# Kernel tuning notes

Hardware: AMD Instinct MI355X
Metric: run time of the kernel (lower is better)

Reference implementation:

```python
import jax, jax.numpy as jnp
import numpy as np

HIDDEN = 1024
N_HEADS = 16
N_LAYERS = 10
LOCAL_K = 3
TOKEN_T, TOKEN_H, TOKEN_W = 4, 16, 16
PATCH_SIZE = 2
LATENT_C = 16
TOKEN_DIM = LATENT_C * PATCH_SIZE * PATCH_SIZE  # 64
TOKEN_IN = TOKEN_DIM + 1                        # 65
N_TOKENS = TOKEN_T * TOKEN_H * TOKEN_W          # 1024
B = 1
HEAD_DIM = HIDDEN // N_HEADS
LN_EPS = 1e-5


def layer_norm(x, w, b):
    m = x.mean(-1, keepdims=True)
    v = ((x - m) ** 2).mean(-1, keepdims=True)
    return (x - m) * jax.lax.rsqrt(v + LN_EPS) * w + b


def patchify(lat):
    Bx, T, C, H, W = lat.shape
    ph, pw = H // PATCH_SIZE, W // PATCH_SIZE
    x = lat.reshape(Bx, T, C, ph, PATCH_SIZE, pw, PATCH_SIZE)
    x = x.transpose(0, 1, 3, 5, 2, 4, 6)
    return x.reshape(Bx, T * ph * pw, C * PATCH_SIZE * PATCH_SIZE)


def unpatchify(tok):
    Bx = tok.shape[0]
    C = TOKEN_DIM // (PATCH_SIZE * PATCH_SIZE)
    x = tok.reshape(Bx, TOKEN_T, TOKEN_H, TOKEN_W, C, PATCH_SIZE, PATCH_SIZE)
    x = x.transpose(0, 1, 4, 2, 5, 3, 6)
    return x.reshape(Bx, TOKEN_T, C, TOKEN_H * PATCH_SIZE, TOKEN_W * PATCH_SIZE)


def gather_neighbors(kv):
    # kv: (B, N, 2D) -> (B, N, 27, 2D), 3x3x3 zero-padded neighborhoods
    Bx, Nx, D2 = kv.shape
    pad = LOCAL_K // 2
    x = kv.reshape(Bx, TOKEN_T, TOKEN_H, TOKEN_W, D2)
    x = jnp.pad(x, ((0, 0), (pad, pad), (pad, pad), (pad, pad), (0, 0)))
    sl = [x[:, dt:dt + TOKEN_T, dh:dh + TOKEN_H, dw:dw + TOKEN_W]
          for dt in range(LOCAL_K) for dh in range(LOCAL_K) for dw in range(LOCAL_K)]
    nb = jnp.stack(sl, axis=4)  # (B,T,H,W,27,2D)
    return nb.reshape(Bx, Nx, LOCAL_K ** 3, D2)


def local_attention(x, qkv_w, out_w):
    Bx, Nx, D = x.shape
    H, d = N_HEADS, HEAD_DIM
    qkv = x @ qkv_w                       # (B,N,3D)
    q, k, v = jnp.split(qkv, 3, axis=-1)
    kv_nb = gather_neighbors(jnp.concatenate([k, v], axis=-1))  # (B,N,27,2D)
    k_nb, v_nb = jnp.split(kv_nb, 2, axis=-1)
    q = q.reshape(Bx, Nx, H, d)
    k_nb = k_nb.reshape(Bx, Nx, LOCAL_K ** 3, H, d)
    v_nb = v_nb.reshape(Bx, Nx, LOCAL_K ** 3, H, d)
    scores = jnp.einsum('bnhd,bnkhd->bnhk', q, k_nb) / np.sqrt(d).astype(np.float32)
    probs = jax.nn.softmax(scores, axis=-1)
    out = jnp.einsum('bnhk,bnkhd->bnhd', probs, v_nb).reshape(Bx, Nx, D)
    return out @ out_w


def global_attention(x, mask_flat, qkv_w, out_w):
    # Each masked query attends to all N keys; math identical to the
    # gather/SDPA/scatter in the original (per-query attention is independent),
    # realized as full attention masked to zero at unmasked positions.
    Bx, Nx, D = x.shape
    H, d = N_HEADS, HEAD_DIM
    qkv = x @ qkv_w
    q, k, v = jnp.split(qkv, 3, axis=-1)
    q = q.reshape(Bx, Nx, H, d)
    k = k.reshape(Bx, Nx, H, d)
    v = v.reshape(Bx, Nx, H, d)
    scores = jnp.einsum('bqhd,bkhd->bhqk', q, k) / np.sqrt(d).astype(np.float32)
    probs = jax.nn.softmax(scores, axis=-1)
    out = jnp.einsum('bhqk,bkhd->bqhd', probs, v).reshape(Bx, Nx, D)
    out = out @ out_w
    return out * mask_flat[..., None].astype(out.dtype)


def setup_inputs() -> dict:
    key = jax.random.key(0)
    ks = jax.random.split(key, 24)
    s = 0.02
    L, D = N_LAYERS, HIDDEN
    inp = {
        'latents': jax.random.normal(ks[0], (B, TOKEN_T, LATENT_C, TOKEN_H * PATCH_SIZE, TOKEN_W * PATCH_SIZE), jnp.float32),
        'token_mask': jax.random.uniform(ks[1], (B, TOKEN_T, TOKEN_H, TOKEN_W)) < 0.1,
        'input_proj_w': jax.random.normal(ks[2], (TOKEN_IN, D), jnp.float32) * s,
        'input_proj_b': jnp.zeros((D,), jnp.float32),
        'emb_t': jax.random.normal(ks[3], (TOKEN_T, D), jnp.float32) * s,
        'emb_h': jax.random.normal(ks[4], (TOKEN_H, D), jnp.float32) * s,
        'emb_w': jax.random.normal(ks[5], (TOKEN_W, D), jnp.float32) * s,
        'ln_local_w': jnp.ones((L, D), jnp.float32),
        'ln_local_b': jnp.zeros((L, D), jnp.float32),
        'ln_global_w': jnp.ones((L, D), jnp.float32),
        'ln_global_b': jnp.zeros((L, D), jnp.float32),
        'ln_ffn_w': jnp.ones((L, D), jnp.float32),
        'ln_ffn_b': jnp.zeros((L, D), jnp.float32),
        'local_qkv_w': jax.random.normal(ks[6], (L, D, 3 * D), jnp.float32) * s,
        'local_out_w': jax.random.normal(ks[7], (L, D, D), jnp.float32) * s,
        'global_qkv_w': jax.random.normal(ks[8], (L, D, 3 * D), jnp.float32) * s,
        'global_out_w': jax.random.normal(ks[9], (L, D, D), jnp.float32) * s,
        'ffn_w1': jax.random.normal(ks[10], (L, D, 4 * D), jnp.float32) * s,
        'ffn_b1': jnp.zeros((L, 4 * D), jnp.float32),
        'ffn_w2': jax.random.normal(ks[11], (L, 4 * D, D), jnp.float32) * s,
        'ffn_b2': jnp.zeros((L, D), jnp.float32),
        'final_ln_w': jnp.ones((D,), jnp.float32),
        'final_ln_b': jnp.zeros((D,), jnp.float32),
        # original zero-inits output_proj; use small random so the test is non-trivial
        'out_proj_w': jax.random.normal(ks[12], (D, TOKEN_DIM), jnp.float32) * s,
        'out_proj_b': jnp.zeros((TOKEN_DIM,), jnp.float32),
    }
    return inp


def reference(latents, token_mask, input_proj_w, input_proj_b, emb_t, emb_h, emb_w,
              ln_local_w, ln_local_b, ln_global_w, ln_global_b, ln_ffn_w, ln_ffn_b,
              local_qkv_w, local_out_w, global_qkv_w, global_out_w,
              ffn_w1, ffn_b1, ffn_w2, ffn_b2, final_ln_w, final_ln_b,
              out_proj_w, out_proj_b):
    Bx = latents.shape[0]
    mask_flat = token_mask.reshape(Bx, -1)
    tokens = patchify(latents)                       # (B, N, TOKEN_DIM)
    flag = mask_flat[..., None].astype(tokens.dtype)
    x = jnp.concatenate([tokens, flag], axis=-1) @ input_proj_w + input_proj_b

    tt, hh, ww = jnp.meshgrid(jnp.arange(TOKEN_T), jnp.arange(TOKEN_H), jnp.arange(TOKEN_W), indexing='ij')
    pos = emb_t[tt.reshape(-1)] + emb_h[hh.reshape(-1)] + emb_w[ww.reshape(-1)]
    x = x + pos[None]

    for l in range(N_LAYERS):
        x = x + local_attention(layer_norm(x, ln_local_w[l], ln_local_b[l]), local_qkv_w[l], local_out_w[l])
        x = x + global_attention(layer_norm(x, ln_global_w[l], ln_global_b[l]), mask_flat, global_qkv_w[l], global_out_w[l])
        h = layer_norm(x, ln_ffn_w[l], ln_ffn_b[l])
        h = jax.nn.gelu(h @ ffn_w1[l] + ffn_b1[l], approximate=False) @ ffn_w2[l] + ffn_b2[l]
        x = x + h

    delta = layer_norm(x, final_ln_w, final_ln_b) @ out_proj_w + out_proj_b
    return unpatchify(tokens + delta)
```

## Files before the change

kernel.cpp:

```cpp
#include <hip/hip_runtime.h>
#include <hip/hip_bf16.h>
#include <math.h>

typedef __bf16 bf16;
typedef __bf16 bf16x8 __attribute__((ext_vector_type(8)));
typedef __bf16 bf16x4 __attribute__((ext_vector_type(4)));
typedef float  f32x4 __attribute__((ext_vector_type(4)));
typedef unsigned int u32x4 __attribute__((ext_vector_type(4)));

#define NTOK 1024
#define HID  1024
#define NH   16
#define HD   64
#define NL   10
#define QCMAX 256

__global__ __launch_bounds__(256)
void wtrans_k(const float* __restrict__ W, bf16* __restrict__ Wt, int K, int N)
{
    __shared__ bf16 tile[64][72];
    const long mofs = (long)blockIdx.z * K * N;
    const float* Ws = W + mofs;
    bf16* Wo = Wt + mofs;
    const int n0 = blockIdx.x * 64, k0 = blockIdx.y * 64;
    const int t = threadIdx.x;
    {
        const int r = t >> 2, cc = (t & 3) * 16;
        const float* src = Ws + (long)(k0 + r) * N + n0 + cc;
#pragma unroll
        for (int i = 0; i < 2; ++i) {
            f32x4 a = *(const f32x4*)(src + i * 8);
            f32x4 b = *(const f32x4*)(src + i * 8 + 4);
            bf16x8 w;
            w[0]=(bf16)a.x; w[1]=(bf16)a.y; w[2]=(bf16)a.z; w[3]=(bf16)a.w;
            w[4]=(bf16)b.x; w[5]=(bf16)b.y; w[6]=(bf16)b.z; w[7]=(bf16)b.w;
            *(bf16x8*)&tile[r][cc + i * 8] = w;
        }
    }
    __syncthreads();
    {
        const int n = t >> 2, kc = (t & 3) * 16;
        bf16x8 o0, o1;
#pragma unroll
        for (int j = 0; j < 8; ++j) { o0[j] = tile[kc + j][n]; o1[j] = tile[kc + 8 + j][n]; }
        bf16* dst = Wo + (long)(n0 + n) * K + k0 + kc;
        *(bf16x8*)dst = o0;
        *(bf16x8*)(dst + 8) = o1;
    }
}

template<int BM, int BN, int KSPLIT>
__global__ __launch_bounds__(256)
void gemm_k(const bf16* __restrict__ A, int lda, long bsA,
            const bf16* __restrict__ Bt, int ldb, long bsB,
            float* __restrict__ Cf, int ldc, long bsC,
            int K)
{
    constexpr int WC  = (BM == 128) ? 2 : 4;
    constexpr int WTN = BN / WC;
    constexpr int NF  = WTN / 16;
    __shared__ bf16 Al[2][BM * 32];
    __shared__ bf16 Bl[2][BN * 32];

    const int t    = threadIdx.x;
    const int lane = t & 63;
    const int wv   = t >> 6;
    const int wr   = wv / WC, wc = wv % WC;
    const int lrow = lane & 15, lk = lane >> 4;
    const int n0   = blockIdx.x * BN;
    const int m0   = blockIdx.y * BM;
    const int ks   = (KSPLIT > 1) ? (blockIdx.z % KSPLIT) : 0;
    const int bz   = (KSPLIT > 1) ? (blockIdx.z / KSPLIT) : blockIdx.z;
    const int Kc   = K / KSPLIT;

    const bf16* Ab = A  + bsA * bz + (long)ks * Kc;
    const bf16* Bb = Bt + bsB * bz + (long)ks * Kc;

    f32x4 acc[4][NF];
#pragma unroll
    for (int m = 0; m < 4; ++m)
#pragma unroll
        for (int n = 0; n < NF; ++n) acc[m][n] = f32x4{0.f, 0.f, 0.f, 0.f};

    const int sr = t >> 2, sc = (t & 3) * 8;

    auto stage = [&](int buf, int kk) {
#pragma unroll
        for (int i = 0; i < BM / 64; ++i)
            __builtin_amdgcn_global_load_lds(
                (const __attribute__((address_space(1))) void*)(Ab + (long)(m0 + sr + i * 64) * lda + kk + sc),
                (__attribute__((address_space(3))) void*)(&Al[buf][i * 2048 + t * 8]), 16, 0, 0);
#pragma unroll
        for (int i = 0; i < BN / 64; ++i)
            __builtin_amdgcn_global_load_lds(
                (const __attribute__((address_space(1))) void*)(Bb + (long)(n0 + sr + i * 64) * ldb + kk + sc),
                (__attribute__((address_space(3))) void*)(&Bl[buf][i * 2048 + t * 8]), 16, 0, 0);
    };

    stage(0, 0);
    __syncthreads();
    int cur = 0;
    for (int k0 = 0; k0 < Kc; k0 += 32) {
        if (k0 + 32 < Kc) stage(cur ^ 1, k0 + 32);
        bf16x8 af[4], bfv[NF];
#pragma unroll
        for (int m = 0; m < 4; ++m)
            af[m] = *(const bf16x8*)&Al[cur][(wr * 64 + m * 16 + lrow) * 32 + lk * 8];
#pragma unroll
        for (int n = 0; n < NF; ++n)
            bfv[n] = *(const bf16x8*)&Bl[cur][(wc * WTN + n * 16 + lrow) * 32 + lk * 8];
#pragma unroll
        for (int m = 0; m < 4; ++m)
#pragma unroll
            for (int n = 0; n < NF; ++n)
                acc[m][n] = __builtin_amdgcn_mfma_f32_16x16x32_bf16(af[m], bfv[n], acc[m][n], 0, 0, 0);
        __syncthreads();
        cur ^= 1;
    }

    float* Co = Cf + bsC * blockIdx.z;
#pragma unroll
    for (int m = 0; m < 4; ++m)
#pragma unroll
        for (int n = 0; n < NF; ++n) {
            const int c = n0 + wc * WTN + n * 16 + lrow;
#pragma unroll
            for (int q = 0; q < 4; ++q) {
                const int r = m0 + wr * 64 + m * 16 + lk * 4 + q;
                Co[(long)r * ldc + c] = acc[m][n][q];
            }
        }
}

template<int NS, bool BIAS, bool SCATTER>
__global__ __launch_bounds__(256)
void ln_add_k(float* __restrict__ x, const float* __restrict__ parts, long pstride,
              const float* __restrict__ bias, const int* __restrict__ rmap,
              const float* __restrict__ w, const float* __restrict__ b,
              bf16* __restrict__ o)
{
    int row  = blockIdx.x * 4 + (threadIdx.x >> 6);
    int lane = threadIdx.x & 63;
    f32x4* xr = (f32x4*)(x + (long)row * HID) + lane * 4;
    f32x4 v[4];
#pragma unroll
    for (int i = 0; i < 4; ++i) v[i] = xr[i];

    if (NS > 0) {
        int prow = SCATTER ? rmap[row] : row;
        if (!SCATTER || prow >= 0) {
            const float* pp = parts + (long)prow * 1024 + lane * 16;
#pragma unroll
            for (int ksi = 0; ksi < NS; ++ksi) {
                const f32x4* q = (const f32x4*)(pp + (long)ksi * pstride);
#pragma unroll
                for (int i = 0; i < 4; ++i) v[i] += q[i];
            }
            if (BIAS) {
                const f32x4* bb = (const f32x4*)bias + lane * 4;
#pragma unroll
                for (int i = 0; i < 4; ++i) v[i] += bb[i];
            }
#pragma unroll
            for (int i = 0; i < 4; ++i) xr[i] = v[i];
        }
    }

    float s = 0.f;
#pragma unroll
    for (int i = 0; i < 4; ++i) s += v[i].x + v[i].y + v[i].z + v[i].w;
    for (int m = 32; m; m >>= 1) s += __shfl_xor(s, m);
    float mean = s * (1.f / 1024.f);
    f32x4 d[4];
    float ss = 0.f;
#pragma unroll
    for (int i = 0; i < 4; ++i) {
        d[i] = v[i] - mean;
        ss += d[i].x * d[i].x + d[i].y * d[i].y + d[i].z * d[i].z + d[i].w * d[i].w;
    }
    for (int m = 32; m; m >>= 1) ss += __shfl_xor(ss, m);
    float rs = rsqrtf(ss * (1.f / 1024.f) + 1e-5f);
    const f32x4* wp = (const f32x4*)w + lane * 4;
    const f32x4* bp = (const f32x4*)b + lane * 4;
    bf16x8 o0, o1;
#pragma unroll
    for (int i = 0; i < 4; ++i) {
        f32x4 wv = wp[i], bv = bp[i];
        f32x4 e;
        e.x = d[i].x * rs * wv.x + bv.x; e.y = d[i].y * rs * wv.y + bv.y;
        e.z = d[i].z * rs * wv.z + bv.z; e.w = d[i].w * rs * wv.w + bv.w;
        if (i < 2) { o0[i*4+0]=(bf16)e.x; o0[i*4+1]=(bf16)e.y; o0[i*4+2]=(bf16)e.z; o0[i*4+3]=(bf16)e.w; }
        else       { int k=(i-2)*4; o1[k+0]=(bf16)e.x; o1[k+1]=(bf16)e.y; o1[k+2]=(bf16)e.z; o1[k+3]=(bf16)e.w; }
    }
    bf16* op = o + (long)row * HID + lane * 16;
    *(bf16x8*)op = o0;
    *(bf16x8*)(op + 8) = o1;
}

__global__ __launch_bounds__(256)
void red2_k(const float* __restrict__ p, float* __restrict__ out, int n4)
{
    int i = blockIdx.x * 256 + threadIdx.x;
    const f32x4* a = (const f32x4*)p;
    const f32x4* b = a + n4;
    ((f32x4*)out)[i] = a[i] + b[i];
}

__global__ __launch_bounds__(256)
void red_gelu_k(const float* __restrict__ p, const float* __restrict__ bias,
                bf16* __restrict__ out)
{
    int i = blockIdx.x * 256 + threadIdx.x;
    f32x4 a = ((const f32x4*)p)[i];
    f32x4 c = ((const f32x4*)(p + 4194304))[i];
    f32x4 bb = ((const f32x4*)bias)[i & 1023];
    f32x4 u = a + c + bb;
    bf16x4 o;
    o[0] = (bf16)(0.5f * u.x * (1.f + erff(u.x * 0.70710678118654752f)));
    o[1] = (bf16)(0.5f * u.y * (1.f + erff(u.y * 0.70710678118654752f)));
    o[2] = (bf16)(0.5f * u.z * (1.f + erff(u.z * 0.70710678118654752f)));
    o[3] = (bf16)(0.5f * u.w * (1.f + erff(u.w * 0.70710678118654752f)));
    ((bf16x4*)out)[i] = o;
}

__global__ __launch_bounds__(256)
void red4pv_k(const float* __restrict__ p, bf16* __restrict__ Oc)
{
    int i = blockIdx.x * 256 + threadIdx.x;
    int d4 = (i & 15) * 4;
    int r  = (i >> 4) & 255;
    int h  = i >> 12;
    const float* base = p + (long)(h * 4) * 16384 + r * 64 + d4;
    f32x4 s = *(const f32x4*)base;
    s += *(const f32x4*)(base + 16384);
    s += *(const f32x4*)(base + 32768);
    s += *(const f32x4*)(base + 49152);
    bf16x4 o;
    o[0] = (bf16)s.x; o[1] = (bf16)s.y; o[2] = (bf16)s.z; o[3] = (bf16)s.w;
    *(bf16x4*)(Oc + (long)r * 1024 + h * 64 + d4) = o;
}

__global__ __launch_bounds__(256)
void lattn_k(const float* __restrict__ qkv, bf16* __restrict__ ao)
{
    int w    = blockIdx.x * 4 + (threadIdx.x >> 6);
    int lane = threadIdx.x & 63;
    int n = w >> 4, h = w & 15;
    int tt = n >> 8, hh = (n >> 4) & 15, ww = n & 15;

    int nj = -1;
    float dotv = 0.f;
    if (lane < 27) {
        int dt = lane / 9 - 1, dh = (lane % 9) / 3 - 1, dw = lane % 3 - 1;
        int t2 = tt + dt, h2 = hh + dh, w2 = ww + dw;
        if (t2 >= 0 && t2 < 4 && h2 >= 0 && h2 < 16 && w2 >= 0 && w2 < 16)
            nj = (t2 << 8) | (h2 << 4) | w2;
    }
    if (nj >= 0) {
        const f32x4* qp = (const f32x4*)(qkv + (long)n * 3072 + h * 64);
        const f32x4* kp = (const f32x4*)(qkv + (long)nj * 3072 + 1024 + h * 64);
#pragma unroll
        for (int i = 0; i < 16; ++i) {
            f32x4 q4 = qp[i], k4 = kp[i];
            dotv += q4.x * k4.x + q4.y * k4.y + q4.z * k4.z + q4.w * k4.w;
        }
    }
    float sc = (lane < 27) ? dotv * 0.125f : -3.0e38f;
    float mx = sc;
    for (int m = 32; m; m >>= 1) mx = fmaxf(mx, __shfl_xor(mx, m));
    float e = (lane < 27) ? __expf(sc - mx) : 0.f;
    float s = e;
    for (int m = 32; m; m >>= 1) s += __shfl_xor(s, m);
    float p = e / s;

    float acc = 0.f;
    for (int j = 0; j < 27; ++j) {
        float pj = __shfl(p, j);
        int  njj = __shfl(nj, j);
        if (njj >= 0) acc += pj * qkv[(long)njj * 3072 + 2048 + h * 64 + lane];
    }
    ao[(long)n * 1024 + h * 64 + lane] = (bf16)acc;
}

__global__ void compact_k(const int* __restrict__ mask, int* __restrict__ qidx,
                          int* __restrict__ rmap)
{
    int lane = threadIdx.x;
    int total = 0;
    for (int base = 0; base < 1024; base += 64) {
        int m = (mask[base + lane] != 0) ? 1 : 0;
        unsigned long long bal = __ballot(m);
        int pos = total + (int)__popcll(bal & ((1ull << lane) - 1ull));
        int ok = (m && pos < QCMAX);
        if (ok) qidx[pos] = base + lane;
        rmap[base + lane] = ok ? pos : -1;
        total += (int)__popcll(bal);
    }
    for (int i = total + lane; i < QCMAX; i += 64) qidx[i] = -1;
}

__global__ __launch_bounds__(256)
void qbuild_k(const float* __restrict__ qkv, const int* __restrict__ qidx,
              bf16* __restrict__ Qc)
{
    const int h = blockIdx.y;
    const int t = threadIdx.x;
    const int r = blockIdx.x * 64 + (t >> 2), dc = (t & 3) * 16;
    const int q = qidx[r];
    bf16x8 o0, o1;
    if (q >= 0) {
        const f32x4* src = (const f32x4*)(qkv + (long)q * 3072 + h * 64 + dc);
#pragma unroll
        for (int i = 0; i < 2; ++i) {
            f32x4 a = src[i * 2] * 0.125f, b = src[i * 2 + 1] * 0.125f;
            bf16x8 w;
            w[0]=(bf16)a.x; w[1]=(bf16)a.y; w[2]=(bf16)a.z; w[3]=(bf16)a.w;
            w[4]=(bf16)b.x; w[5]=(bf16)b.y; w[6]=(bf16)b.z; w[7]=(bf16)b.w;
            if (i == 0) o0 = w; else o1 = w;
        }
    } else {
#pragma unroll
        for (int j = 0; j < 8; ++j) { o0[j] = (bf16)0.f; o1[j] = (bf16)0.f; }
    }
    bf16* dst = Qc + (long)h * (QCMAX * 64) + (long)r * 64 + dc;
    *(bf16x8*)dst = o0;
    *(bf16x8*)(dst + 8) = o1;
}

__global__ __launch_bounds__(256)
void kvbuild_k(const float* __restrict__ qkv, bf16* __restrict__ Kh,
               bf16* __restrict__ Vt)
{
    __shared__ bf16 vt[64][72];
    const int h = blockIdx.y;
    const int k0 = blockIdx.x * 64;
    const int t = threadIdx.x;
    {
        const int r = t >> 2, dc = (t & 3) * 16;
        const float* kp = qkv + (long)(k0 + r) * 3072 + 1024 + h * 64 + dc;
        const float* vp = kp + 1024;
        bf16x8 ko0, ko1;
#pragma unroll
        for (int i = 0; i < 2; ++i) {
            f32x4 a = *(const f32x4*)(kp + i * 8);
            f32x4 b = *(const f32x4*)(kp + i * 8 + 4);
            bf16x8 w;
            w[0]=(bf16)a.x; w[1]=(bf16)a.y; w[2]=(bf16)a.z; w[3]=(bf16)a.w;
            w[4]=(bf16)b.x; w[5]=(bf16)b.y; w[6]=(bf16)b.z; w[7]=(bf16)b.w;
            if (i == 0) ko0 = w; else ko1 = w;
        }
        bf16* kd = Kh + (long)h * (NTOK * 64) + (long)(k0 + r) * 64 + dc;
        *(bf16x8*)kd = ko0;
        *(bf16x8*)(kd + 8) = ko1;
#pragma unroll
        for (int i = 0; i < 2; ++i) {
            f32x4 a = *(const f32x4*)(vp + i * 8);
            f32x4 b = *(const f32x4*)(vp + i * 8 + 4);
            bf16x8 w;
            w[0]=(bf16)a.x; w[1]=(bf16)a.y; w[2]=(bf16)a.z; w[3]=(bf16)a.w;
            w[4]=(bf16)b.x; w[5]=(bf16)b.y; w[6]=(bf16)b.z; w[7]=(bf16)b.w;
            *(bf16x8*)&vt[r][dc + i * 8] = w;
        }
    }
    __syncthreads();
    {
        const int d = t >> 2, kc = (t & 3) * 16;
        bf16x8 o0, o1;
#pragma unroll
        for (int j = 0; j < 8; ++j) { o0[j] = vt[kc + j][d]; o1[j] = vt[kc + 8 + j][d]; }
        bf16* dst = Vt + (long)h * (64 * NTOK) + (long)d * NTOK + k0 + kc;
        *(bf16x8*)dst = o0;
        *(bf16x8*)(dst + 8) = o1;
    }
}

__global__ __launch_bounds__(256)
void softmax_k(const float* __restrict__ S, bf16* __restrict__ P)
{
    int row  = blockIdx.x * 4 + (threadIdx.x >> 6);
    int lane = threadIdx.x & 63;
    const f32x4* sp = (const f32x4*)(S + (long)row * 1024) + lane * 4;
    f32x4 v[4];
#pragma unroll
    for (int i = 0; i < 4; ++i) v[i] = sp[i];
    float mx = -3.0e38f;
#pragma unroll
    for (int i = 0; i < 4; ++i)
        mx = fmaxf(mx, fmaxf(fmaxf(v[i].x, v[i].y), fmaxf(v[i].z, v[i].w)));
    for (int m = 32; m; m >>= 1) mx = fmaxf(mx, __shfl_xor(mx, m));
    f32x4 ev[4];
    float sum = 0.f;
#pragma unroll
    for (int i = 0; i < 4; ++i) {
        ev[i].x = __expf(v[i].x - mx); ev[i].y = __expf(v[i].y - mx);
        ev[i].z = __expf(v[i].z - mx); ev[i].w = __expf(v[i].w - mx);
        sum += ev[i].x + ev[i].y + ev[i].z + ev[i].w;
    }
    for (int m = 32; m; m >>= 1) sum += __shfl_xor(sum, m);
    float inv = 1.f / sum;
    bf16x8 o0, o1;
#pragma unroll
    for (int i = 0; i < 4; ++i) {
        f32x4 e = ev[i] * inv;
        if (i < 2) { o0[i*4+0]=(bf16)e.x; o0[i*4+1]=(bf16)e.y; o0[i*4+2]=(bf16)e.z; o0[i*4+3]=(bf16)e.w; }
        else       { int k=(i-2)*4; o1[k+0]=(bf16)e.x; o1[k+1]=(bf16)e.y; o1[k+2]=(bf16)e.z; o1[k+3]=(bf16)e.w; }
    }
    bf16* op = P + (long)row * 1024 + lane * 16;
    *(bf16x8*)op = o0;
    *(bf16x8*)(op + 8) = o1;
}

__global__ __launch_bounds__(256)
void prep_k(const float* __restrict__ lat, const int* __restrict__ mask,
            const float* __restrict__ Wi, const float* __restrict__ bi,
            const float* __restrict__ et, const float* __restrict__ eh,
            const float* __restrict__ ew,
            float* __restrict__ x, float* __restrict__ tokens)
{
    __shared__ float tl[16][65];
    int t = threadIdx.x;
    int n0 = blockIdx.x * 16;
    for (int idx = t; idx < 16 * 65; idx += 256) {
        int ti = idx / 65, d = idx % 65;
        int n = n0 + ti;
        int tt = n >> 8, hh = (n >> 4) & 15, wwi = n & 15;
        float v;
        if (d < 64) {
            int c = d >> 2, ph = (d >> 1) & 1, pw = d & 1;
            v = lat[(((long)tt * 16 + c) * 32 + hh * 2 + ph) * 32 + wwi * 2 + pw];
            tokens[(long)n * 64 + d] = v;
        } else {
            v = mask[n] ? 1.f : 0.f;
        }
        tl[ti][d] = v;
    }
    __syncthreads();
    f32x4 acc[16];
#pragma unroll
    for (int i = 0; i < 16; ++i) acc[i] = f32x4{0.f, 0.f, 0.f, 0.f};
    for (int d = 0; d < 65; ++d) {
        f32x4 wv = *(const f32x4*)(Wi + (long)d * 1024 + t * 4);
#pragma unroll
        for (int ti = 0; ti < 16; ++ti) acc[ti] += tl[ti][d] * wv;
    }
    f32x4 bb = *(const f32x4*)(bi + t * 4);
    for (int ti = 0; ti < 16; ++ti) {
        int n = n0 + ti;
        int tt = n >> 8, hh = (n >> 4) & 15, wwi = n & 15;
        f32x4 pos = *(const f32x4*)(et + (long)tt * 1024 + t * 4)
                  + *(const f32x4*)(eh + (long)hh * 1024 + t * 4)
                  + *(const f32x4*)(ew + (long)wwi * 1024 + t * 4);
        *(f32x4*)(x + (long)n * 1024 + t * 4) = acc[ti] + bb + pos;
    }
}

__global__ __launch_bounds__(256)
void final_k(const bf16* __restrict__ xn, const float* __restrict__ OW,
             const float* __restrict__ ob, const float* __restrict__ tokens,
             float* __restrict__ out)
{
    __shared__ bf16 xl[8][1024];
    __shared__ float part[4][8][64];
    int t = threadIdx.x;
    int n0 = blockIdx.x * 8;
    for (int i = t; i < 1024; i += 256)
        ((u32x4*)xl)[i] = ((const u32x4*)(xn + (long)n0 * 1024))[i];
    __syncthreads();
    int j = t & 63, s = t >> 6;
    float acc[8] = {0.f, 0.f, 0.f, 0.f, 0.f, 0.f, 0.f, 0.f};
    for (int k = s * 256; k < s * 256 + 256; ++k) {
        float w = OW[(long)k * 64 + j];
#pragma unroll
        for (int ti = 0; ti < 8; ++ti) acc[ti] += (float)xl[ti][k] * w;
    }
    for (int ti = 0; ti < 8; ++ti) part[s][ti][j] = acc[ti];
    __syncthreads();
    if (s == 0) {
        for (int ti = 0; ti < 8; ++ti) {
            int n = n0 + ti;
            float v = part[0][ti][j] + part[1][ti][j] + part[2][ti][j] + part[3][ti][j]
                    + ob[j] + tokens[(long)n * 64 + j];
            int tt = n >> 8, hh = (n >> 4) & 15, wwi = n & 15;
            int c = j >> 2, ph = (j >> 1) & 1, pw = j & 1;
            out[(((long)tt * 16 + c) * 32 + hh * 2 + ph) * 32 + wwi * 2 + pw] = v;
        }
    }
}

extern "C" void kernel_launch(void* const* d_in, const int* in_sizes, int n_in,
                              void* d_out, int out_size, void* d_ws, size_t ws_size,
                              hipStream_t stream)
{
    const float* latents = (const float*)d_in[0];
    const int*   mask    = (const int*)d_in[1];
    const float* ipw  = (const float*)d_in[2];
    const float* ipb  = (const float*)d_in[3];
    const float* et   = (const float*)d_in[4];
    const float* eh   = (const float*)d_in[5];
    const float* ew   = (const float*)d_in[6];
    const float* lnlw = (const float*)d_in[7];
    const float* lnlb = (const float*)d_in[8];
    const float* lngw = (const float*)d_in[9];
    const float* lngb = (const float*)d_in[10];
    const float* lnfw = (const float*)d_in[11];
    const float* lnfb = (const float*)d_in[12];
    const float* lqkv = (const float*)d_in[13];
    const float* lout = (const float*)d_in[14];
    const float* gqkv = (const float*)d_in[15];
    const float* gout = (const float*)d_in[16];
    const float* w1   = (const float*)d_in[17];
    const float* b1   = (const float*)d_in[18];
    const float* w2   = (const float*)d_in[19];
    const float* b2   = (const float*)d_in[20];
    const float* flw  = (const float*)d_in[21];
    const float* flb  = (const float*)d_in[22];
    const float* opw  = (const float*)d_in[23];
    const float* opb  = (const float*)d_in[24];

    char* p = (char*)d_ws;
    auto alloc = [&](size_t bytes) { char* r = p; p += (bytes + 255) & ~(size_t)255; return r; };
    float* x      = (float*)alloc((size_t)4 << 20);
    bf16*  xn     = (bf16*)alloc((size_t)2 << 20);
    float* qkv    = (float*)alloc((size_t)12 << 20);
    bf16*  ao     = (bf16*)alloc((size_t)2 << 20);
    bf16*  hbuf   = (bf16*)alloc((size_t)8 << 20);
    float* tokens = (float*)alloc((size_t)256 << 10);
    bf16*  Qc     = (bf16*)alloc((size_t)512 << 10);
    bf16*  Kh     = (bf16*)alloc((size_t)2 << 20);
    bf16*  Vt     = (bf16*)alloc((size_t)2 << 20);
    float* S      = (float*)alloc((size_t)16 << 20);
    bf16*  P      = (bf16*)alloc((size_t)8 << 20);
    bf16*  Oc     = (bf16*)alloc((size_t)512 << 10);
    int*   qidx   = (int*)alloc(4096);
    int*   rmap   = (int*)alloc(4096);
    float* qkvp  = (float*)alloc((size_t)2 * 1024 * 3072 * 4);
    float* loutp = (float*)alloc((size_t)2 * 1024 * 1024 * 4);
    float* goutp = (float*)alloc((size_t)4 * 256 * 1024 * 4);
    float* pvp   = (float*)alloc((size_t)64 * 256 * 64 * 4);
    float* f1p   = (float*)alloc((size_t)2 * 1024 * 4096 * 4);
    float* f2p   = (float*)alloc((size_t)4 * 1024 * 1024 * 4);
    bf16* lqkvT = (bf16*)alloc((size_t)10 * 3072 * 1024 * 2);
    bf16* loutT = (bf16*)alloc((size_t)10 * 1024 * 1024 * 2);
    bf16* gqkvT = (bf16*)alloc((size_t)10 * 3072 * 1024 * 2);
    bf16* goutT = (bf16*)alloc((size_t)10 * 1024 * 1024 * 2);
    bf16* w1T   = (bf16*)alloc((size_t)10 * 4096 * 1024 * 2);
    bf16* w2T   = (bf16*)alloc((size_t)10 * 1024 * 4096 * 2);

    wtrans_k<<<dim3(48, 16, NL), 256, 0, stream>>>(lqkv, lqkvT, 1024, 3072);
    wtrans_k<<<dim3(16, 16, NL), 256, 0, stream>>>(lout, loutT, 1024, 1024);
    wtrans_k<<<dim3(48, 16, NL), 256, 0, stream>>>(gqkv, gqkvT, 1024, 3072);
    wtrans_k<<<dim3(16, 16, NL), 256, 0, stream>>>(gout, goutT, 1024, 1024);
    wtrans_k<<<dim3(64, 16, NL), 256, 0, stream>>>(w1, w1T, 1024, 4096);
    wtrans_k<<<dim3(16, 64, NL), 256, 0, stream>>>(w2, w2T, 4096, 1024);

    prep_k<<<64, 256, 0, stream>>>(latents, mask, ipw, ipb, et, eh, ew, x, tokens);
    compact_k<<<1, 64, 0, stream>>>(mask, qidx, rmap);

    for (int l = 0; l < NL; ++l) {
        const long wq  = (long)l * 3072 * 1024;
        const long wo  = (long)l * 1024 * 1024;
        const long wf1 = (long)l * 4096 * 1024;

        if (l == 0)
            ln_add_k<0, false, false><<<256, 256, 0, stream>>>(
                x, nullptr, 0, nullptr, nullptr, lnlw, lnlb, xn);
        else
            ln_add_k<4, true, false><<<256, 256, 0, stream>>>(
                x, f2p, (long)1024 * 1024, b2 + (l - 1) * 1024, nullptr,
                lnlw + l * HID, lnlb + l * HID, xn);

        gemm_k<128, 128, 2><<<dim3(24, 8, 2), 256, 0, stream>>>(
            xn, 1024, 0, lqkvT + wq, 1024, 0, qkvp, 3072, (long)1024 * 3072, 1024);
        red2_k<<<3072, 256, 0, stream>>>(qkvp, qkv, 1024 * 3072 / 4);
        lattn_k<<<4096, 256, 0, stream>>>(qkv, ao);
        gemm_k<64, 128, 2><<<dim3(8, 16, 2), 256, 0, stream>>>(
            ao, 1024, 0, loutT + wo, 1024, 0, loutp, 1024, (long)1024 * 1024, 1024);

        ln_add_k<2, false, false><<<256, 256, 0, stream>>>(
            x, loutp, (long)1024 * 1024, nullptr, nullptr,
            lngw + l * HID, lngb + l * HID, xn);

        gemm_k<128, 128, 2><<<dim3(24, 8, 2), 256, 0, stream>>>(
            xn, 1024, 0, gqkvT + wq, 1024, 0, qkvp, 3072, (long)1024 * 3072, 1024);
        red2_k<<<3072, 256, 0, stream>>>(qkvp, qkv, 1024 * 3072 / 4);
        qbuild_k<<<dim3(4, 16), 256, 0, stream>>>(qkv, qidx, Qc);
        kvbuild_k<<<dim3(16, 16), 256, 0, stream>>>(qkv, Kh, Vt);
        gemm_k<64, 128, 1><<<dim3(8, 4, 16), 256, 0, stream>>>(
            Qc, 64, (long)256 * 64, Kh, 64, (long)1024 * 64,
            S, 1024, (long)256 * 1024, 64);
        softmax_k<<<1024, 256, 0, stream>>>(S, P);
        gemm_k<64, 64, 4><<<dim3(1, 4, 64), 256, 0, stream>>>(
            P, 1024, (long)256 * 1024, Vt, 1024, (long)64 * 1024,
            pvp, 64, (long)256 * 64, 1024);
        red4pv_k<<<256, 256, 0, stream>>>(pvp, Oc);
        gemm_k<64, 64, 4><<<dim3(16, 4, 4), 256, 0, stream>>>(
            Oc, 1024, 0, goutT + wo, 1024, 0, goutp, 1024, (long)256 * 1024, 1024);

        ln_add_k<4, false, true><<<256, 256, 0, stream>>>(
            x, goutp, (long)256 * 1024, nullptr, rmap,
            lnfw + l * HID, lnfb + l * HID, xn);

        gemm_k<128, 128, 2><<<dim3(32, 8, 2), 256, 0, stream>>>(
            xn, 1024, 0, w1T + wf1, 1024, 0, f1p, 4096, (long)1024 * 4096, 1024);
        red_gelu_k<<<4096, 256, 0, stream>>>(f1p, b1 + l * 4096, hbuf);
        gemm_k<64, 128, 4><<<dim3(8, 16, 4), 256, 0, stream>>>(
            hbuf, 4096, 0, w2T + wf1, 4096, 0, f2p, 1024, (long)1024 * 1024, 4096);
    }

    ln_add_k<4, true, false><<<256, 256, 0, stream>>>(
        x, f2p, (long)1024 * 1024, b2 + 9 * 1024, nullptr, flw, flb, xn);
    final_k<<<128, 256, 0, stream>>>(xn, opw, opb, tokens, (float*)d_out);
}
```

Measured before the change: 2.300 ms.

## Drop split-K for QKV/FFN1 GEMMs, fuse bias+GELU epilogue, merge Q/KV build kernels

The QKV and FFN1 GEMMs now run without split-K, using 64x128 tiles with more blocks, and write their final output directly. This removes the fp32 partial buffers and the separate red2/red_gelu reduction passes. FFN1 gets a templated epilogue that applies bias and exact GELU and stores bf16. The qbuild and kvbuild kernels are merged into one launch, and the global out-projection is changed to split-K of 8 with a larger partial buffer. The cost is fewer K-parallel blocks per GEMM and uncoalesced scalar bf16 stores in the GELU epilogue.

After: 2.225 ms. -3.3%, faster.

```diff
diff --git a/kernel.cpp b/kernel.cpp
--- a/kernel.cpp
+++ b/kernel.cpp
@@ -14,6 +14,9 @@
 #define HD   64
 #define NL   10
 #define QCMAX 256
+
+#define EPI_F32  0
+#define EPI_GELU 1
 
 __global__ __launch_bounds__(256)
 void wtrans_k(const float* __restrict__ W, bf16* __restrict__ Wt, int K, int N)
@@ -49,12 +52,12 @@
     }
 }
 
-template<int BM, int BN, int KSPLIT>
+template<int EPI, int BM, int BN, int KSPLIT>
 __global__ __launch_bounds__(256)
 void gemm_k(const bf16* __restrict__ A, int lda, long bsA,
             const bf16* __restrict__ Bt, int ldb, long bsB,
-            float* __restrict__ Cf, int ldc, long bsC,
-            int K)
+            void* __restrict__ Cv, int ldc, long bsC,
+            const float* __restrict__ bias, int K)
 {
     constexpr int WC  = (BM == 128) ? 2 : 4;
     constexpr int WTN = BN / WC;
@@ -118,7 +121,8 @@
         cur ^= 1;
     }
 
-    float* Co = Cf + bsC * blockIdx.z;
+    float* Cf = (float*)Cv + bsC * blockIdx.z;
+    bf16*  Cb = (bf16*)Cv + bsC * blockIdx.z;
 #pragma unroll
     for (int m = 0; m < 4; ++m)
 #pragma unroll
@@ -127,7 +131,13 @@
 #pragma unroll
             for (int q = 0; q < 4; ++q) {
                 const int r = m0 + wr * 64 + m * 16 + lk * 4 + q;
-                Co[(long)r * ldc + c] = acc[m][n][q];
+                const float v = acc[m][n][q];
+                const long off = (long)r * ldc + c;
+                if (EPI == EPI_F32) Cf[off] = v;
+                else {
+                    float u = v + bias[c];
+                    Cb[off] = (bf16)(0.5f * u * (1.f + erff(u * 0.70710678118654752f)));
+                }
             }
         }
 }
@@ -195,32 +205,6 @@
     bf16* op = o + (long)row * HID + lane * 16;
     *(bf16x8*)op = o0;
     *(bf16x8*)(op + 8) = o1;
-}
-
-__global__ __launch_bounds__(256)
-void red2_k(const float* __restrict__ p, float* __restrict__ out, int n4)
-{
-    int i = blockIdx.x * 256 + threadIdx.x;
-    const f32x4* a = (const f32x4*)p;
-    const f32x4* b = a + n4;
-    ((f32x4*)out)[i] = a[i] + b[i];
-}
-
-__global__ __launch_bounds__(256)
-void red_gelu_k(const float* __restrict__ p, const float* __restrict__ bias,
-                bf16* __restrict__ out)
-{
-    int i = blockIdx.x * 256 + threadIdx.x;
-    f32x4 a = ((const f32x4*)p)[i];
-    f32x4 c = ((const f32x4*)(p + 4194304))[i];
-    f32x4 bb = ((const f32x4*)bias)[i & 1023];
-    f32x4 u = a + c + bb;
-    bf16x4 o;
-    o[0] = (bf16)(0.5f * u.x * (1.f + erff(u.x * 0.70710678118654752f)));
-    o[1] = (bf16)(0.5f * u.y * (1.f + erff(u.y * 0.70710678118654752f)));
-    o[2] = (bf16)(0.5f * u.z * (1.f + erff(u.z * 0.70710678118654752f)));
-    o[3] = (bf16)(0.5f * u.w * (1.f + erff(u.w * 0.70710678118654752f)));
-    ((bf16x4*)out)[i] = o;
 }
 
 __global__ __launch_bounds__(256)
@@ -300,41 +284,36 @@
 }
 
 __global__ __launch_bounds__(256)
-void qbuild_k(const float* __restrict__ qkv, const int* __restrict__ qidx,
-              bf16* __restrict__ Qc)
-{
+void qkvbuild_k(const float* __restrict__ qkv, const int* __restrict__ qidx,
+                bf16* __restrict__ Qc, bf16* __restrict__ Kh, bf16* __restrict__ Vt)
+{
+    __shared__ bf16 vt[64][72];
     const int h = blockIdx.y;
     const int t = threadIdx.x;
-    const int r = blockIdx.x * 64 + (t >> 2), dc = (t & 3) * 16;
-    const int q = qidx[r];
-    bf16x8 o0, o1;
-    if (q >= 0) {
-        const f32x4* src = (const f32x4*)(qkv + (long)q * 3072 + h * 64 + dc);
-#pragma unroll
-        for (int i = 0; i < 2; ++i) {
-            f32x4 a = src[i * 2] * 0.125f, b = src[i * 2 + 1] * 0.125f;
-            bf16x8 w;
-            w[0]=(bf16)a.x; w[1]=(bf16)a.y; w[2]=(bf16)a.z; w[3]=(bf16)a.w;
-            w[4]=(bf16)b.x; w[5]=(bf16)b.y; w[6]=(bf16)b.z; w[7]=(bf16)b.w;
-            if (i == 0) o0 = w; else o1 = w;
-        }
-    } else {
-#pragma unroll
-        for (int j = 0; j < 8; ++j) { o0[j] = (bf16)0.f; o1[j] = (bf16)0.f; }
-    }
-    bf16* dst = Qc + (long)h * (QCMAX * 64) + (long)r * 64 + dc;
-    *(bf16x8*)dst = o0;
-    *(bf16x8*)(dst + 8) = o1;
-}
-
-__global__ __launch_bounds__(256)
-void kvbuild_k(const float* __restrict__ qkv, bf16* __restrict__ Kh,
-               bf16* __restrict__ Vt)
-{
-    __shared__ bf16 vt[64][72];
-    const int h = blockIdx.y;
-    const int k0 = blockIdx.x * 64;
-    const int t = threadIdx.x;
+    if (blockIdx.x < 4) {
+        const int r = blockIdx.x * 64 + (t >> 2), dc = (t & 3) * 16;
+        const int q = qidx[r];
+        bf16x8 o0, o1;
+        if (q >= 0) {
+            const f32x4* src = (const f32x4*)(qkv + (long)q * 3072 + h * 64 + dc);
+#pragma unroll
+            for (int i = 0; i < 2; ++i) {
+                f32x4 a = src[i * 2] * 0.125f, b = src[i * 2 + 1] * 0.125f;
+                bf16x8 w;
+                w[0]=(bf16)a.x; w[1]=(bf16)a.y; w[2]=(bf16)a.z; w[3]=(bf16)a.w;
+                w[4]=(bf16)b.x; w[5]=(bf16)b.y; w[6]=(bf16)b.z; w[7]=(bf16)b.w;
+                if (i == 0) o0 = w; else o1 = w;
+            }
+        } else {
+#pragma unroll
+            for (int j = 0; j < 8; ++j) { o0[j] = (bf16)0.f; o1[j] = (bf16)0.f; }
+        }
+        bf16* dst = Qc + (long)h * (QCMAX * 64) + (long)r * 64 + dc;
+        *(bf16x8*)dst = o0;
+        *(bf16x8*)(dst + 8) = o1;
+        return;
+    }
+    const int k0 = (blockIdx.x - 4) * 64;
     {
         const int r = t >> 2, dc = (t & 3) * 16;
         const float* kp = qkv + (long)(k0 + r) * 3072 + 1024 + h * 64 + dc;
@@ -533,11 +512,9 @@
     bf16*  Oc     = (bf16*)alloc((size_t)512 << 10);
     int*   qidx   = (int*)alloc(4096);
     int*   rmap   = (int*)alloc(4096);
-    float* qkvp  = (float*)alloc((size_t)2 * 1024 * 3072 * 4);
     float* loutp = (float*)alloc((size_t)2 * 1024 * 1024 * 4);
-    float* goutp = (float*)alloc((size_t)4 * 256 * 1024 * 4);
+    float* goutp = (float*)alloc((size_t)8 * 256 * 1024 * 4);
     float* pvp   = (float*)alloc((size_t)64 * 256 * 64 * 4);
-    float* f1p   = (float*)alloc((size_t)2 * 1024 * 4096 * 4);
     float* f2p   = (float*)alloc((size_t)4 * 1024 * 1024 * 4);
     bf16* lqkvT = (bf16*)alloc((size_t)10 * 3072 * 1024 * 2);
     bf16* loutT = (bf16*)alloc((size_t)10 * 1024 * 1024 * 2);
@@ -569,42 +546,38 @@
                 x, f2p, (long)1024 * 1024, b2 + (l - 1) * 1024, nullptr,
                 lnlw + l * HID, lnlb + l * HID, xn);
 
-        gemm_k<128, 128, 2><<<dim3(24, 8, 2), 256, 0, stream>>>(
-            xn, 1024, 0, lqkvT + wq, 1024, 0, qkvp, 3072, (long)1024 * 3072, 1024);
-        red2_k<<<3072, 256, 0, stream>>>(qkvp, qkv, 1024 * 3072 / 4);
+        gemm_k<EPI_F32, 64, 128, 1><<<dim3(24, 16, 1), 256, 0, stream>>>(
+            xn, 1024, 0, lqkvT + wq, 1024, 0, qkv, 3072, 0, nullptr, 1024);
         lattn_k<<<4096, 256, 0, stream>>>(qkv, ao);
-        gemm_k<64, 128, 2><<<dim3(8, 16, 2), 256, 0, stream>>>(
-            ao, 1024, 0, loutT + wo, 1024, 0, loutp, 1024, (long)1024 * 1024, 1024);
+        gemm_k<EPI_F32, 64, 128, 2><<<dim3(8, 16, 2), 256, 0, stream>>>(
+            ao, 1024, 0, loutT + wo, 1024, 0, loutp, 1024, (long)1024 * 1024, nullptr, 1024);
 
         ln_add_k<2, false, false><<<256, 256, 0, stream>>>(
             x, loutp, (long)1024 * 1024, nullptr, nullptr,
             lngw + l * HID, lngb + l * HID, xn);
 
-        gemm_k<128, 128, 2><<<dim3(24, 8, 2), 256, 0, stream>>>(
-            xn, 1024, 0, gqkvT + wq, 1024, 0, qkvp, 3072, (long)1024 * 3072, 1024);
-        red2_k<<<3072, 256, 0, stream>>>(qkvp, qkv, 1024 * 3072 / 4);
-        qbuild_k<<<dim3(4, 16), 256, 0, stream>>>(qkv, qidx, Qc);
-        kvbuild_k<<<dim3(16, 16), 256, 0, stream>>>(qkv, Kh, Vt);
-        gemm_k<64, 128, 1><<<dim3(8, 4, 16), 256, 0, stream>>>(
+        gemm_k<EPI_F32, 64, 128, 1><<<dim3(24, 16, 1), 256, 0, stream>>>(
+            xn, 1024, 0, gqkvT + wq, 1024, 0, qkv, 3072, 0, nullptr, 1024);
+        qkvbuild_k<<<dim3(20, 16), 256, 0, stream>>>(qkv, qidx, Qc, Kh, Vt);
+        gemm_k<EPI_F32, 64, 128, 1><<<dim3(8, 4, 16), 256, 0, stream>>>(
             Qc, 64, (long)256 * 64, Kh, 64, (long)1024 * 64,
-            S, 1024, (long)256 * 1024, 64);
+            S, 1024, (long)256 * 1024, nullptr, 64);
         softmax_k<<<1024, 256, 0, stream>>>(S, P);
-        gemm_k<64, 64, 4><<<dim3(1, 4, 64), 256, 0, stream>>>(
+        gemm_k<EPI_F32, 64, 64, 4><<<dim3(1, 4, 64), 256, 0, stream>>>(
             P, 1024, (long)256 * 1024, Vt, 1024, (long)64 * 1024,
-            pvp, 64, (long)256 * 64, 1024);
+            pvp, 64, (long)256 * 64, nullptr, 1024);
         red4pv_k<<<256, 256, 0, stream>>>(pvp, Oc);
-        gemm_k<64, 64, 4><<<dim3(16, 4, 4), 256, 0, stream>>>(
-            Oc, 1024, 0, goutT + wo, 1024, 0, goutp, 1024, (long)256 * 1024, 1024);
-
-        ln_add_k<4, false, true><<<256, 256, 0, stream>>>(
+        gemm_k<EPI_F32, 64, 128, 8><<<dim3(8, 4, 8), 256, 0, stream>>>(
+            Oc, 1024, 0, goutT + wo, 1024, 0, goutp, 1024, (long)256 * 1024, nullptr, 1024);
+
+        ln_add_k<8, false, true><<<256, 256, 0, stream>>>(
             x, goutp, (long)256 * 1024, nullptr, rmap,
             lnfw + l * HID, lnfb + l * HID, xn);
 
-        gemm_k<128, 128, 2><<<dim3(32, 8, 2), 256, 0, stream>>>(
-            xn, 1024, 0, w1T + wf1, 1024, 0, f1p, 4096, (long)1024 * 4096, 1024);
-        red_gelu_k<<<4096, 256, 0, stream>>>(f1p, b1 + l * 4096, hbuf);
-        gemm_k<64, 128, 4><<<dim3(8, 16, 4), 256, 0, stream>>>(
-            hbuf, 4096, 0, w2T + wf1, 4096, 0, f2p, 1024, (long)1024 * 1024, 4096);
+        gemm_k<EPI_GELU, 64, 128, 1><<<dim3(32, 16, 1), 256, 0, stream>>>(
+            xn, 1024, 0, w1T + wf1, 1024, 0, hbuf, 4096, 0, b1 + l * 4096, 1024);
+        gemm_k<EPI_F32, 64, 128, 4><<<dim3(8, 16, 4), 256, 0, stream>>>(
+            hbuf, 4096, 0, w2T + wf1, 4096, 0, f2p, 1024, (long)1024 * 1024, nullptr, 4096);
     }
 
     ln_add_k<4, true, false><<<256, 256, 0, stream>>>(
```
